# Performance work log

Measured on AMD Instinct MI355X. Metric: run time of the kernel, lower is better.

The kernel has to match this reference:

```python
import jax, jax.numpy as jnp
import numpy as np

B, N, C, H, BS = 4, 4096, 1024, 16, 64
E = C // H          # head dim = 64
EPS = 1e-3

def setup_inputs() -> dict:
    key = jax.random.key(0)
    k0, k1, k2, k3 = jax.random.split(key, 4)
    x = jax.random.normal(k0, (B, N, C), jnp.float32)
    qkv_w = jax.random.normal(k1, (3 * C, C), jnp.float32) * 0.02
    proj_w = jax.random.normal(k2, (C, C), jnp.float32) * 0.02
    proj_b = jax.random.normal(k3, (C,), jnp.float32) * 0.02
    return {"x": x, "qkv_w": qkv_w, "proj_w": proj_w, "proj_b": proj_b}

def reference(x, qkv_w, proj_w, proj_b):
    b, n, c = x.shape
    h, e, bs = H, E, BS
    u = n // bs  # number of buckets
    # qkv projection (no bias), split to (B,H,N,e) per q/k/v
    qkv = (x @ qkv_w.T).reshape(b, n, 3, h, e).transpose(2, 0, 3, 1, 4)
    q, k, v = qkv[0], qkv[1], qkv[2]
    # feature maps: softmax(q) scaled, exp(k)
    q = jax.nn.softmax(q, axis=-1) * (e ** -0.5)
    k = jnp.exp(k)
    # bucket along sequence: (B,H,U,BS,e)
    b_q = q.reshape(b, h, u, bs, e)
    b_k = k.reshape(b, h, u, bs, e)
    b_v = v.reshape(b, h, u, bs, e)
    # per-bucket k sums and inter-bucket cumulative sums
    b_k_cumsum = jnp.cumsum(b_k.sum(axis=-2), axis=-2)            # (B,H,U,e)
    context = jnp.einsum('bhund,bhune->bhude', b_k, b_v)          # (B,H,U,e,e)
    context = jnp.cumsum(context, axis=2)
    # exclusive shift by one bucket (bucket_size > 1 path in original)
    context = jnp.concatenate(
        [jnp.zeros_like(context[:, :, :1]), context[:, :, :-1]], axis=2)
    b_k_cumsum = jnp.concatenate(
        [jnp.zeros_like(b_k_cumsum[:, :, :1]), b_k_cumsum[:, :, :-1]], axis=2)
    # normalizer, clamped from below at eps
    D_inv = 1.0 / jnp.maximum(
        jnp.einsum('bhud,bhund->bhun', b_k_cumsum, b_q), EPS)
    attn = jnp.einsum('bhund,bhude,bhun->bhune', b_q, context, D_inv)
    out = attn.reshape(b, h, n, e).transpose(0, 2, 1, 3).reshape(b, n, c)
    # output projection (dropouts are identity at eval)
    return out @ proj_w.T + proj_b
```

## Files before the change

kernel.cpp:

```cpp
#include <hip/hip_runtime.h>
#include <stdint.h>


typedef unsigned short u16;
typedef unsigned int u32;
typedef u16   u16x4  __attribute__((ext_vector_type(4)));
typedef u16   u16x8  __attribute__((ext_vector_type(8)));
typedef float f32x4  __attribute__((ext_vector_type(4)));
typedef float float4v __attribute__((ext_vector_type(4)));
typedef __bf16 bf16x8 __attribute__((ext_vector_type(8)));

__device__ __forceinline__ u16 f2bf(float f) {
  return __builtin_bit_cast(u16, (__bf16)f);
}
__device__ __forceinline__ float bf2f(u16 h) {
  return (float)__builtin_bit_cast(__bf16, h);
}

__device__ __forceinline__ void stage16(const u16* g, u16* l) {
  __builtin_amdgcn_global_load_lds(
      (const __attribute__((address_space(1))) u32*)g,
      (__attribute__((address_space(3))) u32*)l, 16, 0, 0);
}

__global__ __launch_bounds__(256) void cvt_all(
    const float* __restrict__ x, const float* __restrict__ wqf,
    const float* __restrict__ wpf, u16* __restrict__ xb,
    u16* __restrict__ wq, u16* __restrict__ wp) {
  int i = blockIdx.x * 256 + threadIdx.x;
  const float* in; u16* out; int j;
  if (i < 4194304)      { in = x;   out = xb; j = i; }
  else if (i < 4980736) { in = wqf; out = wq; j = i - 4194304; }
  else                  { in = wpf; out = wp; j = i - 4980736; }
  float4v v = reinterpret_cast<const float4v*>(in)[j];
  u16x4 o;
  o.x = f2bf(v.x); o.y = f2bf(v.y); o.z = f2bf(v.z); o.w = f2bf(v.w);
  reinterpret_cast<u16x4*>(out)[j] = o;
}

template <int EPI>
__global__ __launch_bounds__(512, 2) void gemm256(
    const u16* __restrict__ A,
    const u16* __restrict__ B,
    const float* __restrict__ bias,
    float* __restrict__ Cf,
    u16* __restrict__ Qf, u16* __restrict__ Kt, u16* __restrict__ Vt,
    float* __restrict__ ksum,
    int N, int K, int NT) {
  __shared__ u16 As[2][2][256][32];
  __shared__ u16 Bs[2][2][256][32];
  const int tid = threadIdx.x, lane = tid & 63, wave = tid >> 6;
  const int wm = wave >> 2, wn = wave & 3;
  const int l15 = lane & 15, l4 = lane >> 4;
  const int ntn = N >> 8;
  const int cpx = gridDim.x >> 3;
  const int bid = (blockIdx.x & 7) * cpx + (blockIdx.x >> 3);
  const int bm = bid / ntn, bn = bid % ntn;

  const int srow = tid >> 2;
  const int gsl8 = ((tid & 3) ^ ((tid >> 3) & 3)) * 8;
  const u16* Ag = A + (size_t)(bm * 256 + srow) * K + gsl8;
  const u16* Bg = B + (size_t)(bn * 256 + srow) * K + gsl8;
  const size_t rj = (size_t)128 * K;
  const int slotr = (l4 ^ ((l15 >> 1) & 3)) * 8;

  f32x4 acc[8][4] = {};
  bf16x8 a0, a1, a2, a3, a4, a5, a6, a7, b0, b1, b2, b3;

#define STG(P, buf, kh, kt)                                        \
  { const u16* g_ = P##g + (kt) + (kh) * 32;                       \
    stage16(g_,      &P##s[buf][kh][wave * 16][0]);                \
    stage16(g_ + rj, &P##s[buf][kh][128 + wave * 16][0]); }

#define LDA(r0_, r1_, r2_, r3_, kk, mh)                                  \
  { const u16* p_ = &As[cur][kk][wm * 128 + (mh) * 64 + l15][0] + slotr; \
    r0_ = *(const bf16x8*)(p_);                                          \
    r1_ = *(const bf16x8*)(p_ + 512);                                    \
    r2_ = *(const bf16x8*)(p_ + 1024);                                   \
    r3_ = *(const bf16x8*)(p_ + 1536); }

#define LDB(kk)                                                    \
  { const u16* p_ = &Bs[cur][kk][wn * 64 + l15][0] + slotr;        \
    b0 = *(const bf16x8*)(p_);                                     \
    b1 = *(const bf16x8*)(p_ + 512);                               \
    b2 = *(const bf16x8*)(p_ + 1024);                              \
    b3 = *(const bf16x8*)(p_ + 1536); }

#define MM(x, y, z) z = __builtin_amdgcn_mfma_f32_16x16x32_bf16(x, y, z, 0, 0, 0)
#define MFMA16(mb, x0, x1, x2, x3)                                 \
  __builtin_amdgcn_s_setprio(1);                                   \
  MM(x0, b0, acc[(mb) + 0][0]); MM(x0, b1, acc[(mb) + 0][1]);      \
  MM(x0, b2, acc[(mb) + 0][2]); MM(x0, b3, acc[(mb) + 0][3]);      \
  MM(x1, b0, acc[(mb) + 1][0]); MM(x1, b1, acc[(mb) + 1][1]);      \
  MM(x1, b2, acc[(mb) + 1][2]); MM(x1, b3, acc[(mb) + 1][3]);      \
  MM(x2, b0, acc[(mb) + 2][0]); MM(x2, b1, acc[(mb) + 2][1]);      \
  MM(x2, b2, acc[(mb) + 2][2]); MM(x2, b3, acc[(mb) + 2][3]);      \
  MM(x3, b0, acc[(mb) + 3][0]); MM(x3, b1, acc[(mb) + 3][1]);      \
  MM(x3, b2, acc[(mb) + 3][2]); MM(x3, b3, acc[(mb) + 3][3]);      \
  __builtin_amdgcn_s_setprio(0);

#define BARF()                                                     \
  { asm volatile("" ::: "memory");                                 \
    __builtin_amdgcn_s_barrier();                                  \
    asm volatile("" ::: "memory"); }

  STG(A, 0, 0, 0) STG(B, 0, 0, 0) STG(A, 0, 1, 0) STG(B, 0, 1, 0)
  asm volatile("s_waitcnt vmcnt(0)" ::: "memory");
  __builtin_amdgcn_s_barrier();
  asm volatile("" ::: "memory");

  for (int t = 0; t < NT; ++t) {
    const int cur = t & 1, nxt = cur ^ 1;
    const int ktn = (t + 1) << 6;
    const bool pre = (t + 1 < NT);
    LDB(0)
    LDA(a0, a1, a2, a3, 0, 0)
    LDA(a4, a5, a6, a7, 0, 1)
    if (pre) STG(A, nxt, 0, ktn)
    MFMA16(0, a0, a1, a2, a3)
    if (pre) STG(B, nxt, 0, ktn)
    MFMA16(4, a4, a5, a6, a7)
    if (pre) { asm volatile("s_waitcnt vmcnt(4)" ::: "memory"); }
    else     { asm volatile("s_waitcnt vmcnt(0)" ::: "memory"); }
    BARF()
    LDB(1)
    LDA(a0, a1, a2, a3, 1, 0)
    LDA(a4, a5, a6, a7, 1, 1)
    if (pre) STG(A, nxt, 1, ktn)
    MFMA16(0, a0, a1, a2, a3)
    if (pre) STG(B, nxt, 1, ktn)
    MFMA16(4, a4, a5, a6, a7)
    if (pre) { asm volatile("s_waitcnt vmcnt(4)" ::: "memory"); }
    BARF()
  }
#undef STG
#undef LDA
#undef LDB
#undef MM
#undef MFMA16
#undef BARF

  const int row0 = bm * 256 + wm * 128 + l4 * 4;
  const int col0 = bn * 256 + wn * 64 + l15;
  if constexpr (EPI == 0) {
    float bv[4];
#pragma unroll
    for (int ni = 0; ni < 4; ++ni) bv[ni] = bias[col0 + ni * 16];
#pragma unroll
    for (int mi = 0; mi < 8; ++mi)
#pragma unroll
      for (int i = 0; i < 4; ++i) {
        size_t r = (size_t)(row0 + mi * 16 + i) * N;
#pragma unroll
        for (int ni = 0; ni < 4; ++ni)
          Cf[r + col0 + ni * 16] = acc[mi][ni][i] + bv[ni];
      }
  } else {
    const int i3 = bn >> 2;
    const int h  = ((bn & 3) << 2) + wn;
    if (i3 == 0) {
#pragma unroll
      for (int mi = 0; mi < 8; ++mi)
#pragma unroll
        for (int i = 0; i < 4; ++i) {
          const int row = row0 + mi * 16 + i;
          const int bb = row >> 12, uu = (row >> 6) & 63, nn = row & 63;
          u16* op = Qf + ((size_t)((bb * 16 + h) * 64 + uu)) * 4096
                        + nn * 64 + l15;
          float v0 = acc[mi][0][i], v1 = acc[mi][1][i];
          float v2 = acc[mi][2][i], v3 = acc[mi][3][i];
          float mx = fmaxf(fmaxf(v0, v1), fmaxf(v2, v3));
          mx = fmaxf(mx, __shfl_xor(mx, 1));
          mx = fmaxf(mx, __shfl_xor(mx, 2));
          mx = fmaxf(mx, __shfl_xor(mx, 4));
          mx = fmaxf(mx, __shfl_xor(mx, 8));
          float e0 = __expf(v0 - mx), e1 = __expf(v1 - mx);
          float e2 = __expf(v2 - mx), e3 = __expf(v3 - mx);
          float s = e0 + e1 + e2 + e3;
          s += __shfl_xor(s, 1); s += __shfl_xor(s, 2);
          s += __shfl_xor(s, 4); s += __shfl_xor(s, 8);
          float inv = 0.125f / s;
          op[0]  = f2bf(e0 * inv); op[16] = f2bf(e1 * inv);
          op[32] = f2bf(e2 * inv); op[48] = f2bf(e3 * inv);
        }
    } else if (i3 == 1) {
      float sk0[4] = {0.f, 0.f, 0.f, 0.f};
      float sk1[4] = {0.f, 0.f, 0.f, 0.f};
#pragma unroll
      for (int mi = 0; mi < 8; ++mi) {
        const int row = row0 + mi * 16;
        const int bb = row >> 12, uu = (row >> 6) & 63, nn = row & 63;
        u16* op = Kt + ((size_t)((bb * 16 + h) * 64 + uu)) * 4096 + nn;
#pragma unroll
        for (int ni = 0; ni < 4; ++ni) {
          float e0 = __expf(acc[mi][ni][0]);
          float e1 = __expf(acc[mi][ni][1]);
          float e2 = __expf(acc[mi][ni][2]);
          float e3 = __expf(acc[mi][ni][3]);
          u16x4 o;
          o.x = f2bf(e0); o.y = f2bf(e1); o.z = f2bf(e2); o.w = f2bf(e3);
          *reinterpret_cast<u16x4*>(op + (ni * 16 + l15) * 64) = o;
          if (mi < 4) sk0[ni] += e0 + e1 + e2 + e3;
          else        sk1[ni] += e0 + e1 + e2 + e3;
        }
      }
#pragma unroll
      for (int ni = 0; ni < 4; ++ni) {
        sk0[ni] += __shfl_xor(sk0[ni], 16); sk0[ni] += __shfl_xor(sk0[ni], 32);
        sk1[ni] += __shfl_xor(sk1[ni], 16); sk1[ni] += __shfl_xor(sk1[ni], 32);
      }
      if (lane < 16) {
        const int nb0 = bm * 256 + wm * 128;
        const size_t bkt0 = (size_t)(((nb0 >> 12) * 16 + h) * 64 + ((nb0 >> 6) & 63));
#pragma unroll
        for (int ni = 0; ni < 4; ++ni) {
          ksum[bkt0 * 64 + ni * 16 + l15]       = sk0[ni];
          ksum[(bkt0 + 1) * 64 + ni * 16 + l15] = sk1[ni];
        }
      }
    } else {
#pragma unroll
      for (int mi = 0; mi < 8; ++mi) {
        const int row = row0 + mi * 16;
        const int bb = row >> 12, uu = (row >> 6) & 63, nn = row & 63;
        u16* op = Vt + ((size_t)((bb * 16 + h) * 64 + uu)) * 4096 + nn;
#pragma unroll
        for (int ni = 0; ni < 4; ++ni) {
          u16x4 o;
          o.x = f2bf(acc[mi][ni][0]); o.y = f2bf(acc[mi][ni][1]);
          o.z = f2bf(acc[mi][ni][2]); o.w = f2bf(acc[mi][ni][3]);
          *reinterpret_cast<u16x4*>(op + (ni * 16 + l15) * 64) = o;
        }
      }
    }
  }
}

__global__ __launch_bounds__(256) void scanctx2(
    const u16* __restrict__ Kt,
    const u16* __restrict__ Vt,
    u16* __restrict__ ctxb,
    float* __restrict__ ksum) {
  const int bh = blockIdx.x >> 2, ec = blockIdx.x & 3;
  const int tid = threadIdx.x, lane = tid & 63, wave = tid >> 6;
  const int l15 = lane & 15, l4 = lane >> 4;
  __shared__ u16 KtL[2][2][64][72];
  __shared__ u16 VtL[2][2][16][72];

  const size_t bbase = (size_t)bh * 64 * 4096;
  const int kr0 = tid >> 3, ks = (tid & 7) * 8;
  const int kr1 = 32 + kr0;
  const bool dov = tid < 128;
  const int vr = tid >> 3, vs = (tid & 7) * 8;
  const bool dok = (ec == 0) && (tid < 64);
  float* kp = dok ? (ksum + (size_t)bh * 4096 + tid) : nullptr;

  f32x4 acc = {0.f, 0.f, 0.f, 0.f};
  u16x8 ka0, ka1, kb0, kb1, va = {}, vb = {};
  float kc0 = 0.f, kc1 = 0.f, kn0 = 0.f, kn1 = 0.f, krun = 0.f;

#define GLD(u_, kx0, kx1, vx)                                          \
  { const size_t nb = bbase + (size_t)(u_) * 4096;                     \
    kx0 = *reinterpret_cast<const u16x8*>(Kt + nb + kr0 * 64 + ks);    \
    kx1 = *reinterpret_cast<const u16x8*>(Kt + nb + kr1 * 64 + ks);    \
    if (dov) vx = *reinterpret_cast<const u16x8*>(                     \
        Vt + nb + (ec * 16 + vr) * 64 + vs); }
#define LWR(buf, j, kx0, kx1, vx)                                      \
  { *reinterpret_cast<u16x8*>(&KtL[buf][j][kr0][ks]) = kx0;            \
    *reinterpret_cast<u16x8*>(&KtL[buf][j][kr1][ks]) = kx1;            \
    if (dov) *reinterpret_cast<u16x8*>(&VtL[buf][j][vr][vs]) = vx; }
#define ACC(buf, j)                                                    \
  _Pragma("unroll")                                                    \
  for (int kk = 0; kk < 2; ++kk) {                                     \
    bf16x8 av = *reinterpret_cast<const bf16x8*>(                      \
        &VtL[buf][j][l15][kk * 32 + l4 * 8]);                          \
    bf16x8 bk = *reinterpret_cast<const bf16x8*>(                      \
        &KtL[buf][j][wave * 16 + l15][kk * 32 + l4 * 8]);              \
    acc = __builtin_amdgcn_mfma_f32_16x16x32_bf16(av, bk, acc, 0, 0, 0); }

  GLD(0, ka0, ka1, va) GLD(1, kb0, kb1, vb)
  if (dok) { kc0 = kp[0]; kc1 = kp[64]; }
  LWR(0, 0, ka0, ka1, va) LWR(0, 1, kb0, kb1, vb)
  __syncthreads();

  for (int u = 0; u < 64; u += 2) {
    const int cur = (u >> 1) & 1, nxt = cur ^ 1;
    const bool pre = (u + 2 < 64);
    if (pre) {
      GLD(u + 2, ka0, ka1, va) GLD(u + 3, kb0, kb1, vb)
      if (dok) { kn0 = kp[(size_t)(u + 2) * 64]; kn1 = kp[(size_t)(u + 3) * 64]; }
    }
    if (dok) {
      kp[(size_t)u * 64] = krun;       krun += kc0;
      kp[(size_t)(u + 1) * 64] = krun; krun += kc1;
      kc0 = kn0; kc1 = kn1;
    }
    u16* cb0 = ctxb + bbase + (size_t)u * 4096 + wave * 16 + l15;
#pragma unroll
    for (int i = 0; i < 4; ++i) cb0[(ec * 16 + l4 * 4 + i) * 64] = f2bf(acc[i]);
    ACC(cur, 0)
    u16* cb1 = cb0 + 4096;
#pragma unroll
    for (int i = 0; i < 4; ++i) cb1[(ec * 16 + l4 * 4 + i) * 64] = f2bf(acc[i]);
    ACC(cur, 1)
    if (pre) { LWR(nxt, 0, ka0, ka1, va) LWR(nxt, 1, kb0, kb1, vb) }
    __syncthreads();
  }
#undef GLD
#undef LWR
#undef ACC
}

__global__ __launch_bounds__(256) void apply(
    const u16* __restrict__ Q, const u16* __restrict__ ctxc,
    const float* __restrict__ kcum, u16* __restrict__ AT) {
  const int bid = blockIdx.x;
  const int u = bid & 63, bh = bid >> 6, b = bh >> 4, h = bh & 15;
  const int tid = threadIdx.x, lane = tid & 63, wave = tid >> 6;
  const int l15 = lane & 15, l4 = lane >> 4;
  __shared__ float kc[64];

  const size_t base = (size_t)bid * 4096;
  if (tid < 64) kc[tid] = kcum[(size_t)bid * 64 + tid];
  __syncthreads();

  bf16x8 aq[2];
  float dpart = 0.f;
#pragma unroll
  for (int kk = 0; kk < 2; ++kk) {
    aq[kk] = *reinterpret_cast<const bf16x8*>(
        Q + base + (wave * 16 + l15) * 64 + kk * 32 + l4 * 8);
    const float* kcp = &kc[kk * 32 + l4 * 8];
#pragma unroll
    for (int j = 0; j < 8; ++j) dpart += (float)aq[kk][j] * kcp[j];
  }
  dpart += __shfl_xor(dpart, 16);
  dpart += __shfl_xor(dpart, 32);
  const float dinv_self = 1.f / fmaxf(dpart, 1e-3f);
  float dv[4];
#pragma unroll
  for (int i = 0; i < 4; ++i) dv[i] = __shfl(dinv_self, l4 * 4 + i);

  f32x4 acc[4] = {};
  const u16* Cu = ctxc + base;
#pragma unroll
  for (int kk = 0; kk < 2; ++kk)
#pragma unroll
    for (int ni = 0; ni < 4; ++ni) {
      bf16x8 bc = *reinterpret_cast<const bf16x8*>(
          Cu + (ni * 16 + l15) * 64 + kk * 32 + l4 * 8);
      acc[ni] = __builtin_amdgcn_mfma_f32_16x16x32_bf16(aq[kk], bc, acc[ni], 0, 0, 0);
    }
  const size_t orow = ((size_t)b * 4096 + u * 64 + wave * 16 + l4 * 4) * 1024 + h * 64;
#pragma unroll
  for (int i = 0; i < 4; ++i) {
#pragma unroll
    for (int ni = 0; ni < 4; ++ni)
      AT[orow + (size_t)i * 1024 + ni * 16 + l15] = f2bf(acc[ni][i] * dv[i]);
  }
}

extern "C" void kernel_launch(void* const* d_in, const int* in_sizes, int n_in,
                              void* d_out, int out_size, void* d_ws, size_t ws_size,
                              hipStream_t stream) {
  (void)in_sizes; (void)n_in; (void)out_size; (void)ws_size;
  const float* x      = (const float*)d_in[0];
  const float* qkv_w  = (const float*)d_in[1];
  const float* proj_w = (const float*)d_in[2];
  const float* proj_b = (const float*)d_in[3];
  float* out = (float*)d_out;

  char* ws = (char*)d_ws;
  u16* xb    = (u16*)(ws);
  u16* wq    = (u16*)(ws + 33554432);
  u16* wp    = (u16*)(ws + 39845888);
  u16* Qf    = (u16*)(ws + 41943040);
  u16* Kt    = (u16*)(ws + 75497472);
  u16* Vt    = (u16*)(ws + 109051904);
  u16* ctxb  = (u16*)(ws + 142606336);
  float* ksum = (float*)(ws + 176160768);
  u16* AT    = Kt;

  cvt_all<<<dim3(20480), dim3(256), 0, stream>>>(x, qkv_w, proj_w, xb, wq, wp);

  gemm256<2><<<dim3(64 * 12), dim3(512), 0, stream>>>(
      xb, wq, nullptr, nullptr, Qf, Kt, Vt, ksum, 3072, 1024, 16);
  scanctx2<<<dim3(256), dim3(256), 0, stream>>>(Kt, Vt, ctxb, ksum);
  apply<<<dim3(4096), dim3(256), 0, stream>>>(Qf, ctxb, ksum, AT);
  gemm256<0><<<dim3(64 * 4), dim3(512), 0, stream>>>(
      AT, wp, proj_b, out, nullptr, nullptr, nullptr, nullptr, 1024, 1024, 16);
}
```

Before: 235.4 us.

## Restructure GEMM mainloop into finer-grained half-tile prefetch pipeline; widen convert kernel

The GEMM main loop now issues LDS reads and MFMAs in four quarter-phases, each separated by barriers. Global-to-LDS staging is interleaved at half-K granularity, so one half-stage is prefetched further ahead, and only four A registers are live instead of eight. This is meant to cut register pressure and overlap global loads with compute more evenly, at the cost of extra barriers and lgkmcnt waits. The convert kernel also processes 8 floats per thread, halving its grid size.

```diff
diff --git a/kernel.cpp b/kernel.cpp
--- a/kernel.cpp
+++ b/kernel.cpp
@@ -29,13 +29,15 @@
     u16* __restrict__ wq, u16* __restrict__ wp) {
   int i = blockIdx.x * 256 + threadIdx.x;
   const float* in; u16* out; int j;
-  if (i < 4194304)      { in = x;   out = xb; j = i; }
-  else if (i < 4980736) { in = wqf; out = wq; j = i - 4194304; }
-  else                  { in = wpf; out = wp; j = i - 4980736; }
-  float4v v = reinterpret_cast<const float4v*>(in)[j];
-  u16x4 o;
-  o.x = f2bf(v.x); o.y = f2bf(v.y); o.z = f2bf(v.z); o.w = f2bf(v.w);
-  reinterpret_cast<u16x4*>(out)[j] = o;
+  if (i < 2097152)      { in = x;   out = xb; j = i; }
+  else if (i < 2490368) { in = wqf; out = wq; j = i - 2097152; }
+  else                  { in = wpf; out = wp; j = i - 2490368; }
+  float4v v0 = reinterpret_cast<const float4v*>(in)[j * 2];
+  float4v v1 = reinterpret_cast<const float4v*>(in)[j * 2 + 1];
+  u16x8 o;
+  o[0] = f2bf(v0.x); o[1] = f2bf(v0.y); o[2] = f2bf(v0.z); o[3] = f2bf(v0.w);
+  o[4] = f2bf(v1.x); o[5] = f2bf(v1.y); o[6] = f2bf(v1.z); o[7] = f2bf(v1.w);
+  reinterpret_cast<u16x8*>(out)[j] = o;
 }
 
 template <int EPI>
@@ -65,21 +67,21 @@
   const int slotr = (l4 ^ ((l15 >> 1) & 3)) * 8;
 
   f32x4 acc[8][4] = {};
-  bf16x8 a0, a1, a2, a3, a4, a5, a6, a7, b0, b1, b2, b3;
+  bf16x8 a0, a1, a2, a3, b0, b1, b2, b3;
 
 #define STG(P, buf, kh, kt)                                        \
   { const u16* g_ = P##g + (kt) + (kh) * 32;                       \
     stage16(g_,      &P##s[buf][kh][wave * 16][0]);                \
     stage16(g_ + rj, &P##s[buf][kh][128 + wave * 16][0]); }
 
-#define LDA(r0_, r1_, r2_, r3_, kk, mh)                                  \
+#define LDA4(kk, mh)                                                     \
   { const u16* p_ = &As[cur][kk][wm * 128 + (mh) * 64 + l15][0] + slotr; \
-    r0_ = *(const bf16x8*)(p_);                                          \
-    r1_ = *(const bf16x8*)(p_ + 512);                                    \
-    r2_ = *(const bf16x8*)(p_ + 1024);                                   \
-    r3_ = *(const bf16x8*)(p_ + 1536); }
-
-#define LDB(kk)                                                    \
+    a0 = *(const bf16x8*)(p_);                                           \
+    a1 = *(const bf16x8*)(p_ + 512);                                     \
+    a2 = *(const bf16x8*)(p_ + 1024);                                    \
+    a3 = *(const bf16x8*)(p_ + 1536); }
+
+#define LDB4(kk)                                                   \
   { const u16* p_ = &Bs[cur][kk][wn * 64 + l15][0] + slotr;        \
     b0 = *(const bf16x8*)(p_);                                     \
     b1 = *(const bf16x8*)(p_ + 512);                               \
@@ -87,58 +89,64 @@
     b3 = *(const bf16x8*)(p_ + 1536); }
 
 #define MM(x, y, z) z = __builtin_amdgcn_mfma_f32_16x16x32_bf16(x, y, z, 0, 0, 0)
-#define MFMA16(mb, x0, x1, x2, x3)                                 \
+#define MFMA16(mb)                                                 \
   __builtin_amdgcn_s_setprio(1);                                   \
-  MM(x0, b0, acc[(mb) + 0][0]); MM(x0, b1, acc[(mb) + 0][1]);      \
-  MM(x0, b2, acc[(mb) + 0][2]); MM(x0, b3, acc[(mb) + 0][3]);      \
-  MM(x1, b0, acc[(mb) + 1][0]); MM(x1, b1, acc[(mb) + 1][1]);      \
-  MM(x1, b2, acc[(mb) + 1][2]); MM(x1, b3, acc[(mb) + 1][3]);      \
-  MM(x2, b0, acc[(mb) + 2][0]); MM(x2, b1, acc[(mb) + 2][1]);      \
-  MM(x2, b2, acc[(mb) + 2][2]); MM(x2, b3, acc[(mb) + 2][3]);      \
-  MM(x3, b0, acc[(mb) + 3][0]); MM(x3, b1, acc[(mb) + 3][1]);      \
-  MM(x3, b2, acc[(mb) + 3][2]); MM(x3, b3, acc[(mb) + 3][3]);      \
+  MM(a0, b0, acc[(mb) + 0][0]); MM(a0, b1, acc[(mb) + 0][1]);      \
+  MM(a0, b2, acc[(mb) + 0][2]); MM(a0, b3, acc[(mb) + 0][3]);      \
+  MM(a1, b0, acc[(mb) + 1][0]); MM(a1, b1, acc[(mb) + 1][1]);      \
+  MM(a1, b2, acc[(mb) + 1][2]); MM(a1, b3, acc[(mb) + 1][3]);      \
+  MM(a2, b0, acc[(mb) + 2][0]); MM(a2, b1, acc[(mb) + 2][1]);      \
+  MM(a2, b2, acc[(mb) + 2][2]); MM(a2, b3, acc[(mb) + 2][3]);      \
+  MM(a3, b0, acc[(mb) + 3][0]); MM(a3, b1, acc[(mb) + 3][1]);      \
+  MM(a3, b2, acc[(mb) + 3][2]); MM(a3, b3, acc[(mb) + 3][3]);      \
   __builtin_amdgcn_s_setprio(0);
 
 #define BARF()                                                     \
   { asm volatile("" ::: "memory");                                 \
     __builtin_amdgcn_s_barrier();                                  \
     asm volatile("" ::: "memory"); }
+#define LGKM0() asm volatile("s_waitcnt lgkmcnt(0)" ::: "memory");
 
   STG(A, 0, 0, 0) STG(B, 0, 0, 0) STG(A, 0, 1, 0) STG(B, 0, 1, 0)
-  asm volatile("s_waitcnt vmcnt(0)" ::: "memory");
+  STG(A, 1, 0, 64) STG(B, 1, 0, 64)
+  asm volatile("s_waitcnt vmcnt(4)" ::: "memory");
   __builtin_amdgcn_s_barrier();
   asm volatile("" ::: "memory");
 
   for (int t = 0; t < NT; ++t) {
-    const int cur = t & 1, nxt = cur ^ 1;
-    const int ktn = (t + 1) << 6;
-    const bool pre = (t + 1 < NT);
-    LDB(0)
-    LDA(a0, a1, a2, a3, 0, 0)
-    LDA(a4, a5, a6, a7, 0, 1)
-    if (pre) STG(A, nxt, 0, ktn)
-    MFMA16(0, a0, a1, a2, a3)
-    if (pre) STG(B, nxt, 0, ktn)
-    MFMA16(4, a4, a5, a6, a7)
-    if (pre) { asm volatile("s_waitcnt vmcnt(4)" ::: "memory"); }
-    else     { asm volatile("s_waitcnt vmcnt(0)" ::: "memory"); }
+    const int cur = t & 1, nx = cur ^ 1;
+    const int k1 = (t + 1) << 6, k2 = (t + 2) << 6;
+    const bool pre1 = (t + 1 < NT), pre2 = (t + 2 < NT);
+    LDB4(0) LDA4(0, 0)
+    if (pre1) STG(A, nx, 1, k1)
+    BARF() LGKM0()
+    MFMA16(0)
     BARF()
-    LDB(1)
-    LDA(a0, a1, a2, a3, 1, 0)
-    LDA(a4, a5, a6, a7, 1, 1)
-    if (pre) STG(A, nxt, 1, ktn)
-    MFMA16(0, a0, a1, a2, a3)
-    if (pre) STG(B, nxt, 1, ktn)
-    MFMA16(4, a4, a5, a6, a7)
-    if (pre) { asm volatile("s_waitcnt vmcnt(4)" ::: "memory"); }
+    LDA4(0, 1)
+    if (pre1) STG(B, nx, 1, k1)
+    BARF() LGKM0()
+    MFMA16(4)
+    BARF()
+    LDB4(1) LDA4(1, 0)
+    if (pre2) STG(A, cur, 0, k2)
+    BARF() LGKM0()
+    MFMA16(0)
+    BARF()
+    LDA4(1, 1)
+    if (pre2) STG(B, cur, 0, k2)
+    BARF() LGKM0()
+    MFMA16(4)
+    if (pre2)      { asm volatile("s_waitcnt vmcnt(4)" ::: "memory"); }
+    else if (pre1) { asm volatile("s_waitcnt vmcnt(0)" ::: "memory"); }
     BARF()
   }
 #undef STG
-#undef LDA
-#undef LDB
+#undef LDA4
+#undef LDB4
 #undef MM
 #undef MFMA16
 #undef BARF
+#undef LGKM0
 
   const int row0 = bm * 256 + wm * 128 + l4 * 4;
   const int col0 = bn * 256 + wn * 64 + l15;
@@ -381,7 +389,7 @@
   float* ksum = (float*)(ws + 176160768);
   u16* AT    = Kt;
 
-  cvt_all<<<dim3(20480), dim3(256), 0, stream>>>(x, qkv_w, proj_w, xb, wq, wp);
+  cvt_all<<<dim3(10240), dim3(256), 0, stream>>>(x, qkv_w, proj_w, xb, wq, wp);
 
   gemm256<2><<<dim3(64 * 12), dim3(512), 0, stream>>>(
       xb, wq, nullptr, nullptr, Qf, Kt, Vt, ksum, 3072, 1024, 16);
```

Result: slower. 245.4 us (+4.3%).
